# Optimization experiments

Hardware: AMD Instinct MI355X
Metric: run time of the kernel (lower is better)

## Reference

```python
import jax, jax.numpy as jnp
import numpy as np

HEADS = 16

def _split_qkv(qkv, h):
    # faithful to rearrange 'b t (d k h) -> k b h t d' with k=3
    b, t, e3 = qkv.shape
    d = e3 // (3 * h)
    qkv = qkv.reshape(b, t, d, 3, h)          # (b,t,d,k,h), d-major packing
    qkv = jnp.transpose(qkv, (3, 0, 4, 1, 2))  # (k,b,h,t,d)
    return qkv[0], qkv[1], qkv[2]

def setup_inputs() -> dict:
    key = jax.random.key(0)
    ks = jax.random.split(key, 5)
    b, t, e = 2, 2048, 1024
    s = e ** -0.5
    return {
        "x": jax.random.normal(ks[0], (b, t, e), jnp.float32),
        "tx": jax.random.normal(ks[1], (b, t, e), jnp.float32),
        "Wqkv": jax.random.normal(ks[2], (3 * e, e), jnp.float32) * s,
        "Wtqkv": jax.random.normal(ks[3], (3 * e, e), jnp.float32) * s,
        "Wout": jax.random.normal(ks[4], (e, e), jnp.float32) * s,
    }

def reference(x, tx, Wqkv, Wtqkv, Wout):
    h = HEADS
    e = x.shape[-1]
    d_head = e // h
    scale = jnp.float32(d_head ** 0.5)  # NOTE: module MULTIPLIES by sqrt(d_head)

    qkv = x @ Wqkv.T     # (b,t,3e)
    tqkv = tx @ Wtqkv.T  # (b,t,3e)
    _q, k, v = _split_qkv(qkv, h)      # each (b,h,t,d)
    tq, _tk, _tv = _split_qkv(tqkv, h)

    energy = jnp.einsum('bhid,bhjd->bhij', tq, k) * scale  # (b,h,t,t)
    attn = jax.nn.softmax(energy, axis=-1)
    out = jnp.einsum('bhij,bhjd->bhid', attn, v)           # (b,h,t,d)
    b, _, t, d = out.shape
    out = jnp.transpose(out, (0, 2, 1, 3)).reshape(b, t, h * d)  # 'b h t d -> b t (h d)'
    return out @ Wout.T
```

## Files before the change

kernel.cpp:

```cpp
#include <hip/hip_runtime.h>

typedef unsigned short u16;
typedef unsigned int u32;
typedef __attribute__((ext_vector_type(8))) short short8;
typedef __attribute__((ext_vector_type(4))) float f32x4;

__device__ inline u16 f32_to_bf16(float f) {
  u32 u = __float_as_uint(f);
  u += 0x7fffu + ((u >> 16) & 1u);
  return (u16)(u >> 16);
}
__device__ inline float bf16_to_f32(u16 s) {
  return __uint_as_float(((u32)s) << 16);
}

#if __has_builtin(__builtin_amdgcn_exp2f)
#define EXP2F(x) __builtin_amdgcn_exp2f(x)
#else
#define EXP2F(x) exp2f(x)
#endif

__device__ inline void dma16(const void* gp, void* lp) {
  __builtin_amdgcn_global_load_lds(
      (const __attribute__((address_space(1))) u32*)gp,
      (__attribute__((address_space(3))) u32*)lp, 16, 0, 0);
}

__device__ inline u32 pack_hi16(u32 a, u32 b) {
  return __builtin_amdgcn_perm(b, a, 0x07060302u);
}
__device__ inline uint4 pack_bf16_8(const uint4 a, const uint4 b) {
  uint4 r;
  r.x = pack_hi16(a.x, a.y);
  r.y = pack_hi16(a.z, a.w);
  r.z = pack_hi16(b.x, b.y);
  r.w = pack_hi16(b.z, b.w);
  return r;
}
__device__ inline void split8(const uint4 a, const uint4 b, uint4& hi, uint4& lo) {
  u32 u[8] = {a.x, a.y, a.z, a.w, b.x, b.y, b.z, b.w};
  u32 l[8];
#pragma unroll
  for (int j = 0; j < 8; ++j)
    l[j] = __float_as_uint(__uint_as_float(u[j]) - __uint_as_float(u[j] & 0xffff0000u));
  hi.x = pack_hi16(u[0], u[1]); hi.y = pack_hi16(u[2], u[3]);
  hi.z = pack_hi16(u[4], u[5]); hi.w = pack_hi16(u[6], u[7]);
  lo.x = pack_hi16(l[0], l[1]); lo.y = pack_hi16(l[2], l[3]);
  lo.z = pack_hi16(l[4], l[5]); lo.w = pack_hi16(l[6], l[7]);
}

__global__ void repack_w(const float* __restrict__ Wqkv, const float* __restrict__ Wtqkv,
                         const float* __restrict__ Wout,
                         u16* __restrict__ Wtq_hi, u16* __restrict__ Wtq_lo,
                         u16* __restrict__ Wk_hi,  u16* __restrict__ Wk_lo,
                         u16* __restrict__ Wv_hi,  u16* __restrict__ Woutb) {
  int r = blockIdx.x;
  int part = r >> 10;
  int rr = r & 1023;
  int h = rr >> 6, d = rr & 63;
  const float* src;
  u16 *dh, *dl = nullptr;
  if (part == 0)      { src = Wtqkv + (size_t)(d * 48 + h) * 1024;      dh = Wtq_hi + (size_t)rr * 1024; dl = Wtq_lo + (size_t)rr * 1024; }
  else if (part == 1) { src = Wqkv  + (size_t)(d * 48 + 16 + h) * 1024; dh = Wk_hi  + (size_t)rr * 1024; dl = Wk_lo  + (size_t)rr * 1024; }
  else if (part == 2) { src = Wqkv  + (size_t)(d * 48 + 32 + h) * 1024; dh = Wv_hi  + (size_t)rr * 1024; }
  else                { src = Wout  + (size_t)rr * 1024;                dh = Woutb  + (size_t)rr * 1024; }
  int c = threadIdx.x * 4;
  f32x4 v = *(const f32x4*)&src[c];
  u32 hv[4], lv[4];
#pragma unroll
  for (int j = 0; j < 4; ++j) {
    u16 hb = f32_to_bf16(v[j]);
    hv[j] = hb;
    lv[j] = f32_to_bf16(v[j] - bf16_to_f32(hb));
  }
  uint2 ho; ho.x = hv[0] | (hv[1] << 16); ho.y = hv[2] | (hv[3] << 16);
  *(uint2*)&dh[c] = ho;
  if (dl) {
    uint2 lo; lo.x = lv[0] | (lv[1] << 16); lo.y = lv[2] | (lv[3] << 16);
    *(uint2*)&dl[c] = lo;
  }
}

__global__ __launch_bounds__(256) __attribute__((amdgpu_waves_per_eu(2)))
void proj_fused(const float* __restrict__ x, const float* __restrict__ tx,
                const u16* __restrict__ Wtq_hi, const u16* __restrict__ Wtq_lo,
                const u16* __restrict__ Wk_hi,  const u16* __restrict__ Wk_lo,
                const u16* __restrict__ Wv_hi,
                u16* __restrict__ Qhi, u16* __restrict__ Qlo,
                u16* __restrict__ Khi, u16* __restrict__ Klo,
                u16* __restrict__ Vt, float qscale) {
  __shared__ __align__(16) float Fs[2][128][32];
  __shared__ __align__(16) u16   Hs[2][128][32];
  __shared__ __align__(16) u16   Ls[2][128][32];
  const int tid = threadIdx.x;
  const int wid = tid >> 6, lane = tid & 63;
  const int g = lane >> 4, l16 = lane & 15;
  const int job = blockIdx.y;
  const int tile = blockIdx.x;
  const int wm = (wid & 1) * 64, wn = (wid >> 1) * 64;

  int m0, n0, N, frow0, hrow0;
  const float* Fsrc;
  const u16 *Hsrc;
  const u16 *Lsrc = nullptr;
  if (job == 0) {
    m0 = (tile >> 3) * 128; n0 = (tile & 7) * 128; N = 1024;
    Fsrc = tx; frow0 = m0; Hsrc = Wtq_hi; Lsrc = Wtq_lo; hrow0 = n0;
  } else if (job == 1) {
    m0 = (tile >> 3) * 128; n0 = (tile & 7) * 128; N = 1024;
    Fsrc = x; frow0 = m0; Hsrc = Wk_hi; Lsrc = Wk_lo; hrow0 = n0;
  } else {
    m0 = (tile >> 5) * 128; n0 = (tile & 31) * 128; N = 4096;
    Fsrc = x; frow0 = n0; Hsrc = Wv_hi; hrow0 = m0;
  }

  const int lrow8 = lane >> 3;
  const int gf = (lane & 7) ^ lrow8;
  const int lrow4 = lane >> 2;
  const int gh = (lane & 3) ^ ((lrow4 ^ (lrow4 >> 2)) & 3);

  auto issue_chunk = [&](int k0, int p) {
#pragma unroll
    for (int t = 0; t < 4; ++t) {
      int rb = wid * 32 + t * 8;
      dma16(&Fsrc[(size_t)(frow0 + rb + lrow8) * 1024 + k0 + gf * 4], &Fs[p][rb][0]);
    }
#pragma unroll
    for (int t = 0; t < 2; ++t) {
      int rb = wid * 32 + t * 16;
      size_t ro = (size_t)(hrow0 + rb + lrow4) * 1024 + k0 + gh * 8;
      dma16(&Hsrc[ro], &Hs[p][rb][0]);
      if (job != 2) dma16(&Lsrc[ro], &Ls[p][rb][0]);
    }
  };

  f32x4 acc[4][4];
  const f32x4 zero4 = {0.f, 0.f, 0.f, 0.f};
#pragma unroll
  for (int i = 0; i < 4; ++i)
#pragma unroll
    for (int j = 0; j < 4; ++j) acc[i][j] = zero4;

  const int sw8 = l16 & 7;
  const int sw4 = (l16 ^ (l16 >> 2)) & 3;

  issue_chunk(0, 0);

  for (int k0 = 0; k0 < 1024; k0 += 32) {
    const int p = (k0 >> 5) & 1;
    __syncthreads();
    if (k0 + 32 < 1024) issue_chunk(k0 + 32, p ^ 1);

    if (job != 2) {
      short8 ah[4], al[4], bh4[4], bl4[4];
#pragma unroll
      for (int mi = 0; mi < 4; ++mi) {
        const int R = wm + mi * 16 + l16;
        uint4 u0 = *(const uint4*)&Fs[p][R][((2 * g) ^ sw8) * 4];
        uint4 u1 = *(const uint4*)&Fs[p][R][((2 * g + 1) ^ sw8) * 4];
        uint4 hi, lo;
        split8(u0, u1, hi, lo);
        ah[mi] = *(short8*)&hi;
        al[mi] = *(short8*)&lo;
      }
#pragma unroll
      for (int ni = 0; ni < 4; ++ni) {
        const int R = wn + ni * 16 + l16;
        const int col = (g ^ sw4) * 8;
        bh4[ni] = *(const short8*)&Hs[p][R][col];
        bl4[ni] = *(const short8*)&Ls[p][R][col];
      }
#pragma unroll
      for (int mi = 0; mi < 4; ++mi)
#pragma unroll
        for (int ni = 0; ni < 4; ++ni) {
          acc[mi][ni] = __builtin_amdgcn_mfma_f32_16x16x32_bf16(ah[mi], bh4[ni], acc[mi][ni], 0, 0, 0);
          acc[mi][ni] = __builtin_amdgcn_mfma_f32_16x16x32_bf16(ah[mi], bl4[ni], acc[mi][ni], 0, 0, 0);
          acc[mi][ni] = __builtin_amdgcn_mfma_f32_16x16x32_bf16(al[mi], bh4[ni], acc[mi][ni], 0, 0, 0);
        }
    } else {
      short8 av[4], bx[4];
#pragma unroll
      for (int mi = 0; mi < 4; ++mi)
        av[mi] = *(const short8*)&Hs[p][wm + mi * 16 + l16][(g ^ sw4) * 8];
#pragma unroll
      for (int ni = 0; ni < 4; ++ni) {
        const int R = wn + ni * 16 + l16;
        uint4 u0 = *(const uint4*)&Fs[p][R][((2 * g) ^ sw8) * 4];
        uint4 u1 = *(const uint4*)&Fs[p][R][((2 * g + 1) ^ sw8) * 4];
        uint4 t = pack_bf16_8(u0, u1);
        bx[ni] = *(short8*)&t;
      }
#pragma unroll
      for (int mi = 0; mi < 4; ++mi)
#pragma unroll
        for (int ni = 0; ni < 4; ++ni)
          acc[mi][ni] = __builtin_amdgcn_mfma_f32_16x16x32_bf16(av[mi], bx[ni], acc[mi][ni], 0, 0, 0);
    }
  }

  u16* Chi = (job == 0) ? Qhi : ((job == 1) ? Khi : Vt);
  u16* Clo = (job == 0) ? Qlo : Klo;
  float scale = (job == 0) ? qscale : 1.0f;
#pragma unroll
  for (int mi = 0; mi < 4; ++mi)
#pragma unroll
    for (int ni = 0; ni < 4; ++ni) {
      int row = m0 + wm + mi * 16 + g * 4;
      int col = n0 + wn + ni * 16 + l16;
#pragma unroll
      for (int r = 0; r < 4; ++r) {
        float v = acc[mi][ni][r] * scale;
        size_t o = (size_t)(row + r) * N + col;
        u32 uv = __float_as_uint(v);
        if (job != 2) {
          Chi[o] = (u16)(uv >> 16);
          float lo = v - __uint_as_float(uv & 0xffff0000u);
          Clo[o] = (u16)(__float_as_uint(lo) >> 16);
        } else {
          Chi[o] = (u16)(uv >> 16);
        }
      }
    }
}

__global__ __launch_bounds__(256) __attribute__((amdgpu_waves_per_eu(2, 4)))
void gemm_out(const u16* __restrict__ A, const u16* __restrict__ B,
              float* __restrict__ C, int M, int N, int K) {
  __shared__ __align__(16) u16 As[128][40];
  __shared__ __align__(16) u16 Bs[64][40];
  const int tid = threadIdx.x;
  const int wid = tid >> 6, lane = tid & 63;
  const int g = lane >> 4, l16 = lane & 15;
  const int m0 = blockIdx.y * 128, n0 = blockIdx.x * 64;
  const int wm = (wid & 1) * 64, wn = (wid >> 1) * 32;

  f32x4 acc[4][2];
  const f32x4 zero4 = {0.f, 0.f, 0.f, 0.f};
#pragma unroll
  for (int i = 0; i < 4; ++i)
#pragma unroll
    for (int j = 0; j < 2; ++j) acc[i][j] = zero4;

  uint4 pa[2], pb;
  const int rowA0 = tid >> 2, colA = (tid & 3) * 8;
  const int rowA1 = rowA0 + 64;
  const int rowB = tid >> 2, colB = (tid & 3) * 8;
  pa[0] = *(const uint4*)&A[(size_t)(m0 + rowA0) * K + colA];
  pa[1] = *(const uint4*)&A[(size_t)(m0 + rowA1) * K + colA];
  pb    = *(const uint4*)&B[(size_t)(n0 + rowB) * K + colB];

  for (int k0 = 0; k0 < K; k0 += 32) {
    __syncthreads();
    *(uint4*)&As[rowA0][colA] = pa[0];
    *(uint4*)&As[rowA1][colA] = pa[1];
    *(uint4*)&Bs[rowB][colB] = pb;
    __syncthreads();
    if (k0 + 32 < K) {
      pa[0] = *(const uint4*)&A[(size_t)(m0 + rowA0) * K + k0 + 32 + colA];
      pa[1] = *(const uint4*)&A[(size_t)(m0 + rowA1) * K + k0 + 32 + colA];
      pb    = *(const uint4*)&B[(size_t)(n0 + rowB) * K + k0 + 32 + colB];
    }
    short8 af[4], bfr[2];
#pragma unroll
    for (int mi = 0; mi < 4; ++mi)
      af[mi] = *(const short8*)&As[wm + mi * 16 + l16][g * 8];
#pragma unroll
    for (int ni = 0; ni < 2; ++ni)
      bfr[ni] = *(const short8*)&Bs[wn + ni * 16 + l16][g * 8];
#pragma unroll
    for (int mi = 0; mi < 4; ++mi)
#pragma unroll
      for (int ni = 0; ni < 2; ++ni)
        acc[mi][ni] = __builtin_amdgcn_mfma_f32_16x16x32_bf16(af[mi], bfr[ni], acc[mi][ni], 0, 0, 0);
  }
#pragma unroll
  for (int mi = 0; mi < 4; ++mi)
#pragma unroll
    for (int ni = 0; ni < 2; ++ni) {
      int row = m0 + wm + mi * 16 + g * 4;
      int col = n0 + wn + ni * 16 + l16;
#pragma unroll
      for (int r = 0; r < 4; ++r)
        C[(size_t)(row + r) * N + col] = acc[mi][ni][r];
    }
}

__global__ __launch_bounds__(512)
void attn_fwd(const u16* __restrict__ Qhi, const u16* __restrict__ Qlo,
              const u16* __restrict__ Khi, const u16* __restrict__ Klo,
              const u16* __restrict__ Vt, u16* __restrict__ O) {
  const int blk = blockIdx.x;
  const int qb = blk & 15, bh = blk >> 4;
  const int h = bh & 15, b = bh >> 4;
  const int t0 = qb * 128;
  const int tid = threadIdx.x, wid = tid >> 6, lane = tid & 63;
  const int g = lane >> 4, l16 = lane & 15;
  const int par = g & 1;
  const int hi2 = g >> 1;

  __shared__ __align__(16) u16 Ksh[2][64][64];
  __shared__ __align__(16) u16 Ksl[2][64][64];
  __shared__ __align__(16) u16 Vs[2][64][64];

  const int lrow = lane >> 3;
  const int lgc  = (lane & 7) ^ lrow;
  const size_t kbase = (size_t)(b * 2048) * 1024 + h * 64;
  const size_t vbase = (size_t)(h * 64) * 4096 + b * 2048;

  auto issue_chunk = [&](int j0, int p) {
    const int row = wid * 8 + lrow;
    dma16(&Khi[kbase + (size_t)(j0 + row) * 1024 + lgc * 8], &Ksh[p][wid * 8][0]);
    dma16(&Klo[kbase + (size_t)(j0 + row) * 1024 + lgc * 8], &Ksl[p][wid * 8][0]);
    dma16(&Vt[vbase + (size_t)row * 4096 + j0 + lgc * 8],    &Vs[p][wid * 8][0]);
  };

  short8 qh[2], ql[2];
#pragma unroll
  for (int ks = 0; ks < 2; ++ks) {
    size_t qo = (size_t)(b * 2048 + t0 + wid * 16 + l16) * 1024
                + h * 64 + ks * 32 + g * 8;
    qh[ks] = *(const short8*)&Qhi[qo];
    ql[ks] = *(const short8*)&Qlo[qo];
  }

  float mrow = -1.0e30f;
  const f32x4 zero4 = {0.f, 0.f, 0.f, 0.f};
  f32x4 acc[5];
#pragma unroll
  for (int dn = 0; dn < 5; ++dn) acc[dn] = zero4;

  short8 ones8;
#pragma unroll
  for (int j = 0; j < 8; ++j) ones8[j] = (short)0x3f80;

  union PB { u32 w[4]; short8 v; };

  issue_chunk(0, 0);

  for (int i = 0; i < 32; ++i) {
    const int p = i & 1;
    __syncthreads();
    if (i < 31) issue_chunk((i + 1) * 64, 1 - p);

    f32x4 s[4];
#pragma unroll
    for (int n = 0; n < 4; ++n) s[n] = zero4;
#pragma unroll
    for (int ks = 0; ks < 2; ++ks)
#pragma unroll
      for (int n = 0; n < 4; ++n) {
        int col = (((ks * 4 + g) ^ (l16 & 7))) * 8;
        short8 kh = *(const short8*)&Ksh[p][n * 16 + l16][col];
        short8 kl = *(const short8*)&Ksl[p][n * 16 + l16][col];
        s[n] = __builtin_amdgcn_mfma_f32_16x16x32_bf16(kh, qh[ks], s[n], 0, 0, 0);
        s[n] = __builtin_amdgcn_mfma_f32_16x16x32_bf16(kh, ql[ks], s[n], 0, 0, 0);
        s[n] = __builtin_amdgcn_mfma_f32_16x16x32_bf16(kl, qh[ks], s[n], 0, 0, 0);
      }

    float cm = -1.0e30f;
#pragma unroll
    for (int n = 0; n < 4; ++n)
#pragma unroll
      for (int r = 0; r < 4; ++r) cm = fmaxf(cm, s[n][r]);
    cm = fmaxf(cm, __shfl_xor(cm, 16));
    cm = fmaxf(cm, __shfl_xor(cm, 32));
    if (!__all(cm <= mrow + 8.0f)) {
      float mnew = fmaxf(mrow, cm);
      float al = EXP2F(mrow - mnew);
      mrow = mnew;
#pragma unroll
      for (int dn = 0; dn < 5; ++dn)
#pragma unroll
        for (int r = 0; r < 4; ++r) acc[dn][r] *= al;
    }

    u32 pk[4][2];
#pragma unroll
    for (int n = 0; n < 4; ++n) {
      float p0 = EXP2F(s[n][0] - mrow);
      float p1 = EXP2F(s[n][1] - mrow);
      float p2 = EXP2F(s[n][2] - mrow);
      float p3 = EXP2F(s[n][3] - mrow);
      pk[n][0] = pack_hi16(__float_as_uint(p0), __float_as_uint(p1));
      pk[n][1] = pack_hi16(__float_as_uint(p2), __float_as_uint(p3));
    }
    PB pb[2];
#pragma unroll
    for (int ks2 = 0; ks2 < 2; ++ks2)
#pragma unroll
      for (int t = 0; t < 4; ++t) {
        int src = (((par << 1) | (t >> 1)) << 4) | l16;
        u32 w0 = (u32)__shfl((int)pk[2 * ks2][t & 1], src);
        u32 w1 = (u32)__shfl((int)pk[2 * ks2 + 1][t & 1], src);
        pb[ks2].w[t] = hi2 ? w1 : w0;
      }

#pragma unroll
    for (int ks2 = 0; ks2 < 2; ++ks2) {
#pragma unroll
      for (int dn = 0; dn < 4; ++dn) {
        int col = (((ks2 * 4 + g) ^ (l16 & 7))) * 8;
        short8 vb = *(const short8*)&Vs[p][dn * 16 + l16][col];
        acc[dn] = __builtin_amdgcn_mfma_f32_16x16x32_bf16(vb, pb[ks2].v, acc[dn], 0, 0, 0);
      }
      acc[4] = __builtin_amdgcn_mfma_f32_16x16x32_bf16(ones8, pb[ks2].v, acc[4], 0, 0, 0);
    }
  }

  float inv = 1.f / acc[4][0];
  int qrow = t0 + wid * 16 + l16;
  size_t base = (size_t)(b * 2048 + qrow) * 1024 + h * 64;
#pragma unroll
  for (int dn = 0; dn < 4; ++dn) {
    u32 o0 = pack_hi16(__float_as_uint(acc[dn][0] * inv),
                       __float_as_uint(acc[dn][1] * inv));
    u32 o1 = pack_hi16(__float_as_uint(acc[dn][2] * inv),
                       __float_as_uint(acc[dn][3] * inv));
    uint2 ov; ov.x = o0; ov.y = o1;
    *(uint2*)&O[base + dn * 16 + g * 4] = ov;
  }
}

extern "C" void kernel_launch(void* const* d_in, const int* in_sizes, int n_in,
                              void* d_out, int out_size, void* d_ws, size_t ws_size,
                              hipStream_t stream) {
  const float* x     = (const float*)d_in[0];
  const float* tx    = (const float*)d_in[1];
  const float* Wqkv  = (const float*)d_in[2];
  const float* Wtqkv = (const float*)d_in[3];
  const float* Wout  = (const float*)d_in[4];
  float* out = (float*)d_out;

  char* ws = (char*)d_ws;
  const size_t MB = 1048576;
  u16* Wtq_hi = (u16*)(ws + 0 * MB);
  u16* Wtq_lo = (u16*)(ws + 2 * MB);
  u16* Wk_hi  = (u16*)(ws + 4 * MB);
  u16* Wk_lo  = (u16*)(ws + 6 * MB);
  u16* Wv_hi  = (u16*)(ws + 8 * MB);
  u16* Woutb  = (u16*)(ws + 10 * MB);
  u16* Qhi    = (u16*)(ws + 12 * MB);
  u16* Qlo    = (u16*)(ws + 20 * MB);
  u16* Khi    = (u16*)(ws + 28 * MB);
  u16* Klo    = (u16*)(ws + 36 * MB);
  u16* Vt     = (u16*)(ws + 44 * MB);
  u16* Ob     = (u16*)(ws + 0 * MB);
  if (ws_size < 52 * MB) return;

  const float QSCALE = 8.0f * 1.4426950408889634f;

  repack_w<<<4096, 256, 0, stream>>>(Wqkv, Wtqkv, Wout,
                                     Wtq_hi, Wtq_lo, Wk_hi, Wk_lo, Wv_hi, Woutb);
  proj_fused<<<dim3(256, 3), 256, 0, stream>>>(x, tx, Wtq_hi, Wtq_lo, Wk_hi, Wk_lo,
                                               Wv_hi, Qhi, Qlo, Khi, Klo, Vt, QSCALE);
  attn_fwd<<<512, 512, 0, stream>>>(Qhi, Qlo, Khi, Klo, Vt, Ob);
  gemm_out<<<dim3(16, 32), 256, 0, stream>>>(Ob, Woutb, out, 4096, 1024, 1024);
}
```

Before: 304.7 us.

## Halve projection tile M to 64 and raise occupancy with job-specific LDS layout

Shrinks the proj_fused output tile from 128x128 to 64x128 per block, doubling the grid to 512x3 blocks, and raises the waves-per-EU hint from 2 to 3. The LDS is now one 48KB byte buffer carved up differently for the hi/lo jobs and the V job, and the DMA issue pattern is rewritten for the smaller tiles. The goal is more blocks in flight and fewer registers per thread (half the accumulators), so more waves can hide memory latency across the 256 CUs. The cost is less operand reuse per block and more total global and LDS traffic for the weight operands.

New measurement: 306.3 us. Within noise of the previous version (+0.6%).

```diff
diff --git a/kernel.cpp b/kernel.cpp
--- a/kernel.cpp
+++ b/kernel.cpp
@@ -81,7 +81,7 @@
   }
 }
 
-__global__ __launch_bounds__(256) __attribute__((amdgpu_waves_per_eu(2)))
+__global__ __launch_bounds__(256) __attribute__((amdgpu_waves_per_eu(3)))
 void proj_fused(const float* __restrict__ x, const float* __restrict__ tx,
                 const u16* __restrict__ Wtq_hi, const u16* __restrict__ Wtq_lo,
                 const u16* __restrict__ Wk_hi,  const u16* __restrict__ Wk_lo,
@@ -89,30 +89,34 @@
                 u16* __restrict__ Qhi, u16* __restrict__ Qlo,
                 u16* __restrict__ Khi, u16* __restrict__ Klo,
                 u16* __restrict__ Vt, float qscale) {
-  __shared__ __align__(16) float Fs[2][128][32];
-  __shared__ __align__(16) u16   Hs[2][128][32];
-  __shared__ __align__(16) u16   Ls[2][128][32];
+  __shared__ __align__(16) char lds[49152];
   const int tid = threadIdx.x;
   const int wid = tid >> 6, lane = tid & 63;
   const int g = lane >> 4, l16 = lane & 15;
   const int job = blockIdx.y;
   const int tile = blockIdx.x;
-  const int wm = (wid & 1) * 64, wn = (wid >> 1) * 64;
+  const int wm = (wid & 1) * 32, wn = (wid >> 1) * 64;
 
   int m0, n0, N, frow0, hrow0;
   const float* Fsrc;
   const u16 *Hsrc;
   const u16 *Lsrc = nullptr;
   if (job == 0) {
-    m0 = (tile >> 3) * 128; n0 = (tile & 7) * 128; N = 1024;
+    m0 = (tile >> 3) * 64; n0 = (tile & 7) * 128; N = 1024;
     Fsrc = tx; frow0 = m0; Hsrc = Wtq_hi; Lsrc = Wtq_lo; hrow0 = n0;
   } else if (job == 1) {
-    m0 = (tile >> 3) * 128; n0 = (tile & 7) * 128; N = 1024;
+    m0 = (tile >> 3) * 64; n0 = (tile & 7) * 128; N = 1024;
     Fsrc = x; frow0 = m0; Hsrc = Wk_hi; Lsrc = Wk_lo; hrow0 = n0;
   } else {
-    m0 = (tile >> 5) * 128; n0 = (tile & 31) * 128; N = 4096;
+    m0 = (tile >> 5) * 64; n0 = (tile & 31) * 128; N = 4096;
     Fsrc = x; frow0 = n0; Hsrc = Wv_hi; hrow0 = m0;
   }
+
+  const int fstride = (job != 2) ? 8192 : 16384;
+  char* const Fb0 = lds;
+  char* const Hb0 = (job != 2) ? (lds + 16384) : (lds + 32768);
+  const int hstride = (job != 2) ? 8192 : 4096;
+  char* const Lb0 = lds + 32768;
 
   const int lrow8 = lane >> 3;
   const int gf = (lane & 7) ^ lrow8;
@@ -120,24 +124,41 @@
   const int gh = (lane & 3) ^ ((lrow4 ^ (lrow4 >> 2)) & 3);
 
   auto issue_chunk = [&](int k0, int p) {
-#pragma unroll
-    for (int t = 0; t < 4; ++t) {
-      int rb = wid * 32 + t * 8;
-      dma16(&Fsrc[(size_t)(frow0 + rb + lrow8) * 1024 + k0 + gf * 4], &Fs[p][rb][0]);
-    }
-#pragma unroll
-    for (int t = 0; t < 2; ++t) {
-      int rb = wid * 32 + t * 16;
-      size_t ro = (size_t)(hrow0 + rb + lrow4) * 1024 + k0 + gh * 8;
-      dma16(&Hsrc[ro], &Hs[p][rb][0]);
-      if (job != 2) dma16(&Lsrc[ro], &Ls[p][rb][0]);
+    if (job != 2) {
+      char* Fb = Fb0 + p * fstride;
+      char* Hb = Hb0 + p * hstride;
+      char* Lb = Lb0 + p * hstride;
+#pragma unroll
+      for (int t = 0; t < 2; ++t) {
+        int rb = wid * 8 + t * 32;
+        dma16(&Fsrc[(size_t)(frow0 + rb + lrow8) * 1024 + k0 + gf * 4], Fb + rb * 128);
+      }
+#pragma unroll
+      for (int t = 0; t < 2; ++t) {
+        int rb = wid * 16 + t * 64;
+        size_t ro = (size_t)(hrow0 + rb + lrow4) * 1024 + k0 + gh * 8;
+        dma16(&Hsrc[ro], Hb + rb * 64);
+        dma16(&Lsrc[ro], Lb + rb * 64);
+      }
+    } else {
+      char* Fb = Fb0 + p * fstride;
+      char* Hb = Hb0 + p * hstride;
+#pragma unroll
+      for (int t = 0; t < 4; ++t) {
+        int rb = wid * 8 + t * 32;
+        dma16(&Fsrc[(size_t)(frow0 + rb + lrow8) * 1024 + k0 + gf * 4], Fb + rb * 128);
+      }
+      {
+        int rb = wid * 16;
+        dma16(&Hsrc[(size_t)(hrow0 + rb + lrow4) * 1024 + k0 + gh * 8], Hb + rb * 64);
+      }
     }
   };
 
-  f32x4 acc[4][4];
+  f32x4 acc[2][4];
   const f32x4 zero4 = {0.f, 0.f, 0.f, 0.f};
 #pragma unroll
-  for (int i = 0; i < 4; ++i)
+  for (int i = 0; i < 2; ++i)
 #pragma unroll
     for (int j = 0; j < 4; ++j) acc[i][j] = zero4;
 
@@ -151,13 +172,16 @@
     __syncthreads();
     if (k0 + 32 < 1024) issue_chunk(k0 + 32, p ^ 1);
 
+    char* Fb = Fb0 + p * fstride;
+    char* Hb = Hb0 + p * hstride;
     if (job != 2) {
-      short8 ah[4], al[4], bh4[4], bl4[4];
-#pragma unroll
-      for (int mi = 0; mi < 4; ++mi) {
+      char* Lb = Lb0 + p * hstride;
+      short8 ah[2], al[2], bh4[4], bl4[4];
+#pragma unroll
+      for (int mi = 0; mi < 2; ++mi) {
         const int R = wm + mi * 16 + l16;
-        uint4 u0 = *(const uint4*)&Fs[p][R][((2 * g) ^ sw8) * 4];
-        uint4 u1 = *(const uint4*)&Fs[p][R][((2 * g + 1) ^ sw8) * 4];
+        uint4 u0 = *(const uint4*)(Fb + R * 128 + ((2 * g) ^ sw8) * 16);
+        uint4 u1 = *(const uint4*)(Fb + R * 128 + ((2 * g + 1) ^ sw8) * 16);
         uint4 hi, lo;
         split8(u0, u1, hi, lo);
         ah[mi] = *(short8*)&hi;
@@ -166,12 +190,11 @@
 #pragma unroll
       for (int ni = 0; ni < 4; ++ni) {
         const int R = wn + ni * 16 + l16;
-        const int col = (g ^ sw4) * 8;
-        bh4[ni] = *(const short8*)&Hs[p][R][col];
-        bl4[ni] = *(const short8*)&Ls[p][R][col];
-      }
-#pragma unroll
-      for (int mi = 0; mi < 4; ++mi)
+        bh4[ni] = *(const short8*)(Hb + R * 64 + (g ^ sw4) * 16);
+        bl4[ni] = *(const short8*)(Lb + R * 64 + (g ^ sw4) * 16);
+      }
+#pragma unroll
+      for (int mi = 0; mi < 2; ++mi)
 #pragma unroll
         for (int ni = 0; ni < 4; ++ni) {
           acc[mi][ni] = __builtin_amdgcn_mfma_f32_16x16x32_bf16(ah[mi], bh4[ni], acc[mi][ni], 0, 0, 0);
@@ -179,20 +202,20 @@
           acc[mi][ni] = __builtin_amdgcn_mfma_f32_16x16x32_bf16(al[mi], bh4[ni], acc[mi][ni], 0, 0, 0);
         }
     } else {
-      short8 av[4], bx[4];
-#pragma unroll
-      for (int mi = 0; mi < 4; ++mi)
-        av[mi] = *(const short8*)&Hs[p][wm + mi * 16 + l16][(g ^ sw4) * 8];
+      short8 av[2], bx[4];
+#pragma unroll
+      for (int mi = 0; mi < 2; ++mi)
+        av[mi] = *(const short8*)(Hb + (wm + mi * 16 + l16) * 64 + (g ^ sw4) * 16);
 #pragma unroll
       for (int ni = 0; ni < 4; ++ni) {
         const int R = wn + ni * 16 + l16;
-        uint4 u0 = *(const uint4*)&Fs[p][R][((2 * g) ^ sw8) * 4];
-        uint4 u1 = *(const uint4*)&Fs[p][R][((2 * g + 1) ^ sw8) * 4];
+        uint4 u0 = *(const uint4*)(Fb + R * 128 + ((2 * g) ^ sw8) * 16);
+        uint4 u1 = *(const uint4*)(Fb + R * 128 + ((2 * g + 1) ^ sw8) * 16);
         uint4 t = pack_bf16_8(u0, u1);
         bx[ni] = *(short8*)&t;
       }
 #pragma unroll
-      for (int mi = 0; mi < 4; ++mi)
+      for (int mi = 0; mi < 2; ++mi)
 #pragma unroll
         for (int ni = 0; ni < 4; ++ni)
           acc[mi][ni] = __builtin_amdgcn_mfma_f32_16x16x32_bf16(av[mi], bx[ni], acc[mi][ni], 0, 0, 0);
@@ -203,7 +226,7 @@
   u16* Clo = (job == 0) ? Qlo : Klo;
   float scale = (job == 0) ? qscale : 1.0f;
 #pragma unroll
-  for (int mi = 0; mi < 4; ++mi)
+  for (int mi = 0; mi < 2; ++mi)
 #pragma unroll
     for (int ni = 0; ni < 4; ++ni) {
       int row = m0 + wm + mi * 16 + g * 4;
@@ -452,7 +475,7 @@
 
   repack_w<<<4096, 256, 0, stream>>>(Wqkv, Wtqkv, Wout,
                                      Wtq_hi, Wtq_lo, Wk_hi, Wk_lo, Wv_hi, Woutb);
-  proj_fused<<<dim3(256, 3), 256, 0, stream>>>(x, tx, Wtq_hi, Wtq_lo, Wk_hi, Wk_lo,
+  proj_fused<<<dim3(512, 3), 256, 0, stream>>>(x, tx, Wtq_hi, Wtq_lo, Wk_hi, Wk_lo,
                                                Wv_hi, Qhi, Qlo, Khi, Klo, Vt, QSCALE);
   attn_fwd<<<512, 512, 0, stream>>>(Qhi, Qlo, Khi, Klo, Vt, Ob);
   gemm_out<<<dim3(16, 32), 256, 0, stream>>>(Ob, Woutb, out, 4096, 1024, 1024);
```

## Double-buffer output GEMM with direct global-to-LDS DMA and swizzled LDS reads

Applied to the files above, without the earlier changes.

The output-projection GEMM now loads tiles with global_load_lds DMA straight into a double-buffered LDS array, instead of staging them through registers. The next K-chunk is issued while the current one is being consumed, so there is one barrier per iteration instead of two. An XOR swizzle on the 16-byte column groups replaces the padded rows to avoid LDS bank conflicts. The waves_per_eu hint is removed. Correctness depends on the DMA for buffer p having completed at the barrier, and only the smaller output GEMM is touched.

Result: faster. 289.8 us (-4.9%).

```diff
diff --git a/kernel.cpp b/kernel.cpp
--- a/kernel.cpp
+++ b/kernel.cpp
@@ -224,17 +224,32 @@
     }
 }
 
-__global__ __launch_bounds__(256) __attribute__((amdgpu_waves_per_eu(2, 4)))
+__global__ __launch_bounds__(256)
 void gemm_out(const u16* __restrict__ A, const u16* __restrict__ B,
               float* __restrict__ C, int M, int N, int K) {
-  __shared__ __align__(16) u16 As[128][40];
-  __shared__ __align__(16) u16 Bs[64][40];
+  __shared__ __align__(16) u16 As[2][128][32];
+  __shared__ __align__(16) u16 Bs[2][64][32];
   const int tid = threadIdx.x;
   const int wid = tid >> 6, lane = tid & 63;
   const int g = lane >> 4, l16 = lane & 15;
   const int m0 = blockIdx.y * 128, n0 = blockIdx.x * 64;
   const int wm = (wid & 1) * 64, wn = (wid >> 1) * 32;
 
+  const int lrow4 = lane >> 2;
+  const int gh = (lane & 3) ^ ((lrow4 ^ (lrow4 >> 2)) & 3);
+
+  auto issue_chunk = [&](int k0, int p) {
+#pragma unroll
+    for (int t = 0; t < 2; ++t) {
+      int rb = wid * 32 + t * 16;
+      dma16(&A[(size_t)(m0 + rb + lrow4) * K + k0 + gh * 8], &As[p][rb][0]);
+    }
+    {
+      int rb = wid * 16;
+      dma16(&B[(size_t)(n0 + rb + lrow4) * K + k0 + gh * 8], &Bs[p][rb][0]);
+    }
+  };
+
   f32x4 acc[4][2];
   const f32x4 zero4 = {0.f, 0.f, 0.f, 0.f};
 #pragma unroll
@@ -242,32 +257,22 @@
 #pragma unroll
     for (int j = 0; j < 2; ++j) acc[i][j] = zero4;
 
-  uint4 pa[2], pb;
-  const int rowA0 = tid >> 2, colA = (tid & 3) * 8;
-  const int rowA1 = rowA0 + 64;
-  const int rowB = tid >> 2, colB = (tid & 3) * 8;
-  pa[0] = *(const uint4*)&A[(size_t)(m0 + rowA0) * K + colA];
-  pa[1] = *(const uint4*)&A[(size_t)(m0 + rowA1) * K + colA];
-  pb    = *(const uint4*)&B[(size_t)(n0 + rowB) * K + colB];
+  const int sw4 = (l16 ^ (l16 >> 2)) & 3;
+
+  issue_chunk(0, 0);
 
   for (int k0 = 0; k0 < K; k0 += 32) {
+    const int p = (k0 >> 5) & 1;
     __syncthreads();
-    *(uint4*)&As[rowA0][colA] = pa[0];
-    *(uint4*)&As[rowA1][colA] = pa[1];
-    *(uint4*)&Bs[rowB][colB] = pb;
-    __syncthreads();
-    if (k0 + 32 < K) {
-      pa[0] = *(const uint4*)&A[(size_t)(m0 + rowA0) * K + k0 + 32 + colA];
-      pa[1] = *(const uint4*)&A[(size_t)(m0 + rowA1) * K + k0 + 32 + colA];
-      pb    = *(const uint4*)&B[(size_t)(n0 + rowB) * K + k0 + 32 + colB];
-    }
+    if (k0 + 32 < K) issue_chunk(k0 + 32, p ^ 1);
+
     short8 af[4], bfr[2];
 #pragma unroll
     for (int mi = 0; mi < 4; ++mi)
-      af[mi] = *(const short8*)&As[wm + mi * 16 + l16][g * 8];
+      af[mi] = *(const short8*)&As[p][wm + mi * 16 + l16][(g ^ sw4) * 8];
 #pragma unroll
     for (int ni = 0; ni < 2; ++ni)
-      bfr[ni] = *(const short8*)&Bs[wn + ni * 16 + l16][g * 8];
+      bfr[ni] = *(const short8*)&Bs[p][wn + ni * 16 + l16][(g ^ sw4) * 8];
 #pragma unroll
     for (int mi = 0; mi < 4; ++mi)
 #pragma unroll
```
